# Optimization experiments

Measured on AMD Instinct MI355X. Metric: run time of the kernel, lower is better.

## Reference

```python
import jax, jax.numpy as jnp
import numpy as np

B, CIN, N, K, G, COUT = 8, 128, 2048, 16, 4, 256
NL = COUT // 4          # nl_channels = int(0.25*out_channels) = 64
L = COUT - NL           # l_channels = 192
CL = L // G             # 48 per local head
CNL = NL // G           # 16 per non-local head


def setup_inputs() -> dict:
    key = jax.random.key(0)
    ks = jax.random.split(key, 16)
    s = 0.05
    r = lambda k_, sh: s * jax.random.normal(k_, sh, jnp.float32)
    return {
        "x": jax.random.normal(ks[0], (B, CIN, N, K), jnp.float32),
        "abs_x": jax.random.normal(ks[1], (B, CIN // 2, N, 1), jnp.float32),
        "points": jax.random.normal(ks[2], (B, 3, N), jnp.float32),
        "Wq": r(ks[3], (L, CIN // 2)),
        "Wk": r(ks[4], (L, CIN // 2)),
        "Wv": r(ks[5], (L, CIN)),
        "Wnq": r(ks[6], (NL, CIN // 2)),
        "Wnk": r(ks[7], (NL, CIN // 2)),
        "Wnv1": r(ks[8], (NL, CIN // 2)),
        "Wnv2": r(ks[9], (NL, CIN // 2)),
        "pe_w1": r(ks[10], (3, L)),
        "pe_b1": jnp.zeros((L,), jnp.float32),
        "pe_w2": r(ks[11], (L, L)),
        "pe_b2": jnp.zeros((L,), jnp.float32),
        "npe_w1": r(ks[12], (G, 3, CNL)),
        "npe_b1": jnp.zeros((G, CNL), jnp.float32),
        "npe_w2": r(ks[13], (G, CNL, CNL)),
        "npe_b2": jnp.zeros((G, CNL), jnp.float32),
        "idx": jax.random.randint(ks[14], (B, 1, N, K), 0, N, dtype=jnp.int32),
    }


def _forward(x, abs_x, points, Wq, Wk, Wv, Wnq, Wnk, Wnv1, Wnv2,
             pe_w1, pe_b1, pe_w2, pe_b2, npe_w1, npe_b1, npe_w2, npe_b2, idx):
    b, c, n, k = x.shape
    half = c // 2
    idx_sq = idx[:, 0]                                   # (b,n,k)

    # ---- 1. Local attention over kNN neighbors ----
    lq = jnp.einsum('oc,bcns->bons', Wq, abs_x).reshape(b, G, CL, n, 1)
    lk = jnp.einsum('oc,bcnk->bonk', Wk, x[:, half:] + x[:, :half]).reshape(b, G, CL, n, k)
    lv = jnp.einsum('oc,bcnk->bonk', Wv, x).reshape(b, G, CL, n, k)

    # absolute positional encoding (select_neighbors -> carte MLP)
    nbr = jax.vmap(lambda p, i: p[:, i])(points, idx_sq)  # (b,3,n,k)
    rel = nbr - nbr[..., 0:1]                             # subtract first neighbor
    h = jax.nn.relu(jnp.einsum('bcnk,cd->bnkd', rel, pe_w1) + pe_b1)
    pe = (jnp.einsum('bnkd,de->bnke', h, pe_w2) + pe_b2).transpose(0, 3, 1, 2)
    lk = lk + pe.reshape(b, G, CL, n, k)

    att = jax.nn.softmax((lq * lk).sum(2), axis=-1)       # (b,G,n,k)
    local_feature = jnp.einsum('bgnk,bgcnk->bgcn', att, lv).reshape(b, L, n, 1)

    # ---- scatter-based sparse attention centrality + top-k node selection ----
    idx_flat = idx_sq.reshape(b, n * k)
    att_flat = att.reshape(b, G, n * k)

    def scat(a_g, i):  # a_g: (G, n*k), i: (n*k,)
        return jax.vmap(lambda a: jnp.zeros((n,), a.dtype).at[i].add(a))(a_g)

    cent = jax.vmap(scat)(att_flat, idx_flat)             # (b,G,n)
    vals, inds = jax.lax.top_k(cent, k)                   # (b,G,k)

    # ---- 2. Non-local MHA over selected nodes ----
    a2 = abs_x[..., 0]                                    # (b,half,n)
    nq = jnp.einsum('oc,bcn->bon', Wnq, a2).reshape(b, G, CNL, n)
    nk_ = jnp.einsum('oc,bcn->bon', Wnk, a2).reshape(b, G, CNL, n)
    nv1 = jnp.einsum('oc,bcn->bon', Wnv1, a2).reshape(b, G, CNL, n)
    nv2 = jnp.einsum('oc,bcn->bon', Wnv2, a2).reshape(b, G, CNL, n)

    gi = inds[:, :, None, :]                              # (b,G,1,k)
    nk_sel = jnp.take_along_axis(nk_, gi, axis=3)         # (b,G,CNL,k)
    nv2j = jnp.take_along_axis(nv2, gi, axis=3)           # (b,G,CNL,k)

    # per-group non-local positional encoding (constant over n by construction)
    sel = jnp.take_along_axis(jnp.broadcast_to(points[:, None], (b, G, 3, n)), gi, axis=3)  # (b,G,3,k)
    rel_nl = sel - sel[..., 0:1]
    h2 = jax.nn.relu(jnp.einsum('bgck,gcd->bgkd', rel_nl, npe_w1) + npe_b1[None, :, None, :])
    pe_nl = (jnp.einsum('bgkd,gde->bgke', h2, npe_w2) + npe_b2[None, :, None, :]).transpose(0, 1, 3, 2)  # (b,G,CNL,k)

    att_nl = jax.nn.softmax(jnp.einsum('bgcn,bgck->bgnk', nq, nk_sel + pe_nl), axis=-1)
    # value[b,g,c,n,k] = nv1[...,n] - nv2[...,n] + nv2j[...,k], gated by tanh(centrality)
    w = att_nl * jnp.tanh(vals)[:, :, None, :]            # (b,G,n,k)
    s = w.sum(-1)                                         # (b,G,n)
    nl_feature = (nv1 - nv2) * s[:, :, None, :] + jnp.einsum('bgnk,bgck->bgcn', w, nv2j)
    nl_feature = nl_feature.reshape(b, NL, n, 1)

    return jnp.concatenate([local_feature, nl_feature], axis=1)  # (b,COUT,n,1)


def reference(x, abs_x, points, Wq, Wk, Wv, Wnq, Wnk, Wnv1, Wnv2,
              pe_w1, pe_b1, pe_w2, pe_b2, npe_w1, npe_b1, npe_w2, npe_b2, idx):
    return _forward(x, abs_x, points, Wq, Wk, Wv, Wnq, Wnk, Wnv1, Wnv2,
                    pe_w1, pe_b1, pe_w2, pe_b2, npe_w1, npe_b1, npe_w2, npe_b2, idx)
```

## Files before the change

kernel.cpp:

```cpp
#include <hip/hip_runtime.h>
#include <cstddef>

constexpr int NN = 2048;
constexpr int GG = 4;

__global__ __launch_bounds__(256) void prep_q(const float* __restrict__ Wq,
                                              const float* __restrict__ Wk,
                                              const float* __restrict__ pe_w2,
                                              float* __restrict__ Qbuf) {
    const int g = blockIdx.x >> 6, c2 = blockIdx.x & 63;
    const int row = threadIdx.x;
    float acc = 0.f;
    if (row < 64) {
        for (int j = 0; j < 48; ++j) {
            const int o = g * 48 + j;
            acc = fmaf(Wk[o * 64 + row], Wq[o * 64 + c2], acc);
        }
    } else {
        const int d = row - 64;
        for (int j = 0; j < 48; ++j) {
            const int o = g * 48 + j;
            acc = fmaf(pe_w2[(size_t)d * 192 + o], Wq[o * 64 + c2], acc);
        }
    }
    Qbuf[((size_t)(g * 64 + c2) << 8) + row] = acc;
}

__global__ __launch_bounds__(256, 3) void local_v7c(
    const float* __restrict__ x, const float* __restrict__ abs_x,
    const float* __restrict__ points, const float* __restrict__ Wv,
    const float* __restrict__ pe_w1, const float* __restrict__ pe_b1,
    const int* __restrict__ idx, const float* __restrict__ Qbuf,
    float* __restrict__ out, float* __restrict__ cent)
{
    const int bn = blockIdx.x;
    const int b  = bn >> 8;
    const int n0 = (bn & 255) << 3;
    const int tid = threadIdx.x;

    __shared__ int   sidx[128];
    __shared__ float sa2[64][8];
    __shared__ __align__(16) float s_big[4224];
    __shared__ float spart[128][9];
    __shared__ float s_small[544];

    float* sq   = s_big;
    float* sw2  = s_big;
    float* sxw  = s_big;
    float* spts = s_small;
    float* satt = s_small;

    if (tid < 128) sidx[tid] = idx[((size_t)b * NN + n0) * 16 + tid];
    for (int i = tid; i < 512; i += 256) {
        int c = i >> 3, nl = i & 7;
        sa2[c][nl] = abs_x[((size_t)b * 64 + c) * NN + n0 + nl];
    }
    __syncthreads();

    for (int i = tid; i < 384; i += 256) {
        int c3 = i >> 7, r = i & 127;
        spts[(c3 * 8 + (r >> 4)) * 16 + (r & 15)] =
            points[((size_t)b * 3 + c3) * NN + sidx[r]];
    }
    {
        const int g = tid >> 6, row = tid & 63;
        const float* qb = Qbuf + (((size_t)g * 64) << 8) + row;
        float a0 = 0.f, a1 = 0.f, a2v = 0.f, a3 = 0.f,
              a4 = 0.f, a5 = 0.f, a6 = 0.f, a7 = 0.f;
        for (int c2 = 0; c2 < 64; ++c2) {
            const float qv = qb[c2 << 8];
            const float4 v0 = *(const float4*)&sa2[c2][0];
            const float4 v1 = *(const float4*)&sa2[c2][4];
            a0 = fmaf(qv, v0.x, a0); a1 = fmaf(qv, v0.y, a1);
            a2v = fmaf(qv, v0.z, a2v); a3 = fmaf(qv, v0.w, a3);
            a4 = fmaf(qv, v1.x, a4); a5 = fmaf(qv, v1.y, a5);
            a6 = fmaf(qv, v1.z, a6); a7 = fmaf(qv, v1.w, a7);
        }
        const int base = (g << 3) * 65 + row;
        sq[base + 0 * 65] = a0; sq[base + 1 * 65] = a1;
        sq[base + 2 * 65] = a2v; sq[base + 3 * 65] = a3;
        sq[base + 4 * 65] = a4; sq[base + 5 * 65] = a5;
        sq[base + 6 * 65] = a6; sq[base + 7 * 65] = a7;
    }
    __syncthreads();

    const int col = tid & 127, dh = tid >> 7;
    const int nlc = col >> 4, kkc = col & 15;

    {
        const float* xp = x + (((size_t)(b * 128 + dh * 32) * NN) + n0 + nlc) * 16 + kkc;
        const float* q0 = &sq[((0 << 3) + nlc) * 65 + dh * 32];
        const float* q1 = &sq[((1 << 3) + nlc) * 65 + dh * 32];
        const float* q2 = &sq[((2 << 3) + nlc) * 65 + dh * 32];
        const float* q3 = &sq[((3 << 3) + nlc) * 65 + dh * 32];
        float a0 = 0.f, a1 = 0.f, a2v = 0.f, a3 = 0.f;
        for (int i = 0; i < 32; ++i) {
            const float xs = xp[0] + xp[(size_t)64 * NN * 16];
            xp += NN * 16;
            a0 = fmaf(q0[i], xs, a0);
            a1 = fmaf(q1[i], xs, a1);
            a2v = fmaf(q2[i], xs, a2v);
            a3 = fmaf(q3[i], xs, a3);
        }
        spart[col][dh * 4 + 0] = a0; spart[col][dh * 4 + 1] = a1;
        spart[col][dh * 4 + 2] = a2v; spart[col][dh * 4 + 3] = a3;
    }
    __syncthreads();

    const float r0 = spts[(0 * 8 + nlc) * 16 + kkc] - spts[(0 * 8 + nlc) * 16];
    const float r1 = spts[(1 * 8 + nlc) * 16 + kkc] - spts[(1 * 8 + nlc) * 16];
    const float r2 = spts[(2 * 8 + nlc) * 16 + kkc] - spts[(2 * 8 + nlc) * 16];
    #pragma unroll
    for (int p = 0; p < 2; ++p) {
        if (tid < 192) {
            const int d = tid;
            float w00=0.f,w01=0.f,w02=0.f,w03=0.f,w04=0.f,w05=0.f,w06=0.f,w07=0.f;
            float w10=0.f,w11=0.f,w12=0.f,w13=0.f,w14=0.f,w15=0.f,w16=0.f,w17=0.f;
            const float* qb0 = Qbuf + (((size_t)(2 * p + 0) * 64) << 8) + 64 + d;
            const float* qb1 = Qbuf + (((size_t)(2 * p + 1) * 64) << 8) + 64 + d;
            for (int c2 = 0; c2 < 64; ++c2) {
                const float qv0 = qb0[c2 << 8];
                const float qv1 = qb1[c2 << 8];
                const float4 v0 = *(const float4*)&sa2[c2][0];
                const float4 v1 = *(const float4*)&sa2[c2][4];
                w00 = fmaf(qv0, v0.x, w00); w01 = fmaf(qv0, v0.y, w01);
                w02 = fmaf(qv0, v0.z, w02); w03 = fmaf(qv0, v0.w, w03);
                w04 = fmaf(qv0, v1.x, w04); w05 = fmaf(qv0, v1.y, w05);
                w06 = fmaf(qv0, v1.z, w06); w07 = fmaf(qv0, v1.w, w07);
                w10 = fmaf(qv1, v0.x, w10); w11 = fmaf(qv1, v0.y, w11);
                w12 = fmaf(qv1, v0.z, w12); w13 = fmaf(qv1, v0.w, w13);
                w14 = fmaf(qv1, v1.x, w14); w15 = fmaf(qv1, v1.y, w15);
                w16 = fmaf(qv1, v1.z, w16); w17 = fmaf(qv1, v1.w, w17);
            }
            sw2[(0 * 8 + 0) * 196 + d] = w00; sw2[(0 * 8 + 1) * 196 + d] = w01;
            sw2[(0 * 8 + 2) * 196 + d] = w02; sw2[(0 * 8 + 3) * 196 + d] = w03;
            sw2[(0 * 8 + 4) * 196 + d] = w04; sw2[(0 * 8 + 5) * 196 + d] = w05;
            sw2[(0 * 8 + 6) * 196 + d] = w06; sw2[(0 * 8 + 7) * 196 + d] = w07;
            sw2[(1 * 8 + 0) * 196 + d] = w10; sw2[(1 * 8 + 1) * 196 + d] = w11;
            sw2[(1 * 8 + 2) * 196 + d] = w12; sw2[(1 * 8 + 3) * 196 + d] = w13;
            sw2[(1 * 8 + 4) * 196 + d] = w14; sw2[(1 * 8 + 5) * 196 + d] = w15;
            sw2[(1 * 8 + 6) * 196 + d] = w16; sw2[(1 * 8 + 7) * 196 + d] = w17;
        }
        __syncthreads();
        {
            float pB0 = 0.f, pB1 = 0.f;
            const float* w0 = &sw2[(0 * 8 + nlc) * 196];
            const float* w1 = &sw2[(1 * 8 + nlc) * 196];
            const int d0 = dh * 96;
            for (int d = d0; d < d0 + 96; d += 4) {
                const float4 w1a = *(const float4*)&pe_w1[d];
                const float4 w1b = *(const float4*)&pe_w1[192 + d];
                const float4 w1c = *(const float4*)&pe_w1[384 + d];
                const float4 bb  = *(const float4*)&pe_b1[d];
                const float h0 = fmaxf(fmaf(r0, w1a.x, fmaf(r1, w1b.x, fmaf(r2, w1c.x, bb.x))), 0.f);
                const float h1 = fmaxf(fmaf(r0, w1a.y, fmaf(r1, w1b.y, fmaf(r2, w1c.y, bb.y))), 0.f);
                const float h2 = fmaxf(fmaf(r0, w1a.z, fmaf(r1, w1b.z, fmaf(r2, w1c.z, bb.z))), 0.f);
                const float h3 = fmaxf(fmaf(r0, w1a.w, fmaf(r1, w1b.w, fmaf(r2, w1c.w, bb.w))), 0.f);
                const float4 wa = *(const float4*)&w0[d];
                const float4 wb = *(const float4*)&w1[d];
                pB0 = fmaf(h0, wa.x, fmaf(h1, wa.y, fmaf(h2, wa.z, fmaf(h3, wa.w, pB0))));
                pB1 = fmaf(h0, wb.x, fmaf(h1, wb.y, fmaf(h2, wb.z, fmaf(h3, wb.w, pB1))));
            }
            spart[col][dh * 4 + 2 * p + 0] += pB0;
            spart[col][dh * 4 + 2 * p + 1] += pB1;
        }
        __syncthreads();
    }

    if (tid < 32) {
        const int g = tid >> 3, nl = tid & 7;
        float lg[16], m = -1e30f;
        #pragma unroll
        for (int kk = 0; kk < 16; ++kk) {
            const int cc = nl * 16 + kk;
            lg[kk] = spart[cc][g] + spart[cc][4 + g];
            m = fmaxf(m, lg[kk]);
        }
        float s = 0.f;
        #pragma unroll
        for (int kk = 0; kk < 16; ++kk) { lg[kk] = __expf(lg[kk] - m); s += lg[kk]; }
        const float inv = 1.f / s;
        #pragma unroll
        for (int kk = 0; kk < 16; ++kk) satt[nl * 68 + g * 16 + kk] = lg[kk] * inv;
    }
    __syncthreads();

    #pragma unroll
    for (int t = 0; t < 4; ++t) {
        const int i2 = t * 256 + tid;
        const int c = i2 >> 3, nl = i2 & 7;
        const float* xp = x + (((size_t)(b * 128 + c) * NN) + n0 + nl) * 16;
        const float4 x0 = *(const float4*)(xp);
        const float4 x1 = *(const float4*)(xp + 4);
        const float4 x2 = *(const float4*)(xp + 8);
        const float4 x3 = *(const float4*)(xp + 12);
        const float* at = &satt[nl * 68];
        #pragma unroll
        for (int g = 0; g < 4; ++g) {
            const float* a = at + g * 16;
            float v = 0.f;
            v = fmaf(x0.x, a[0],  v); v = fmaf(x0.y, a[1],  v);
            v = fmaf(x0.z, a[2],  v); v = fmaf(x0.w, a[3],  v);
            v = fmaf(x1.x, a[4],  v); v = fmaf(x1.y, a[5],  v);
            v = fmaf(x1.z, a[6],  v); v = fmaf(x1.w, a[7],  v);
            v = fmaf(x2.x, a[8],  v); v = fmaf(x2.y, a[9],  v);
            v = fmaf(x2.z, a[10], v); v = fmaf(x2.w, a[11], v);
            v = fmaf(x3.x, a[12], v); v = fmaf(x3.y, a[13], v);
            v = fmaf(x3.z, a[14], v); v = fmaf(x3.w, a[15], v);
            sxw[((g << 3) + nl) * 132 + c] = v;
        }
    }
    __syncthreads();

    #pragma unroll
    for (int rep = 0; rep < 6; ++rep) {
        const int i = rep * 256 + tid;
        const int o = i >> 3, nl = i & 7;
        const int g = o / 48;
        const float* wv  = Wv + (size_t)o * 128;
        const float* xwp = &sxw[((g << 3) + nl) * 132];
        float a = 0.f;
        for (int c = 0; c < 128; c += 4) {
            const float4 w4  = *(const float4*)(wv + c);
            const float4 xw4 = *(const float4*)(xwp + c);
            a = fmaf(w4.x, xw4.x, fmaf(w4.y, xw4.y, fmaf(w4.z, xw4.z, fmaf(w4.w, xw4.w, a))));
        }
        out[(((size_t)b << 8) + o) * NN + n0 + nl] = a;
    }

    if (tid < 32) {
        const int g = tid >> 3, nl = tid & 7;
        #pragma unroll
        for (int kk = 0; kk < 16; ++kk)
            atomicAdd(&cent[((size_t)(b * GG + g) << 11) + sidx[nl * 16 + kk]],
                      satt[nl * 68 + g * 16 + kk]);
    }
}

__global__ __launch_bounds__(512) void topk_prep_kernel(
    const float* __restrict__ abs_x, const float* __restrict__ points,
    const float* __restrict__ Wnk, const float* __restrict__ Wnv2,
    const float* __restrict__ npe_w1, const float* __restrict__ npe_b1,
    const float* __restrict__ npe_w2, const float* __restrict__ npe_b2,
    const float* __restrict__ cent,
    float* __restrict__ nkpe, float* __restrict__ nv2j, float* __restrict__ tanhv)
{
    const int bg  = blockIdx.x;
    const int b   = bg >> 2, g = bg & 3;
    const int tid = threadIdx.x;
    __shared__ float sc[2048];
    __shared__ float rv[8];  __shared__ int ri[8];
    __shared__ float svals[16]; __shared__ int sinds[16];
    __shared__ float srel[3][16];
    __shared__ float sh2[16][16];

    for (int i = tid; i < 2048; i += 512) sc[i] = cent[((size_t)bg << 11) + i];
    __syncthreads();
    for (int t = 0; t < 16; ++t) {
        float bv = -1e30f; int bi = 1 << 30;
        for (int i = tid; i < 2048; i += 512) {
            float v = sc[i];
            if (v > bv) { bv = v; bi = i; }
        }
        #pragma unroll
        for (int off = 1; off < 64; off <<= 1) {
            float ov = __shfl_xor(bv, off, 64);
            int   oi = __shfl_xor(bi, off, 64);
            if (ov > bv || (ov == bv && oi < bi)) { bv = ov; bi = oi; }
        }
        if ((tid & 63) == 0) { rv[tid >> 6] = bv; ri[tid >> 6] = bi; }
        __syncthreads();
        if (tid == 0) {
            for (int w = 1; w < 8; ++w)
                if (rv[w] > bv || (rv[w] == bv && ri[w] < bi)) { bv = rv[w]; bi = ri[w]; }
            svals[t] = bv; sinds[t] = bi;
            sc[bi] = -1e30f;
        }
        __syncthreads();
    }

    if (tid < 48) {
        int c = tid >> 4, j = tid & 15;
        srel[c][j] = points[((size_t)b * 3 + c) * NN + sinds[j]]
                   - points[((size_t)b * 3 + c) * NN + sinds[0]];
    }
    __syncthreads();
    if (tid < 256) {
        int j = tid >> 4, d = tid & 15;
        float a = npe_b1[g * 16 + d];
        #pragma unroll
        for (int c = 0; c < 3; ++c) a = fmaf(srel[c][j], npe_w1[((g * 3 + c) << 4) + d], a);
        sh2[j][d] = fmaxf(a, 0.f);
    }
    __syncthreads();
    if (tid < 256) {
        int c = tid >> 4, j = tid & 15;
        float a = npe_b2[g * 16 + c];
        #pragma unroll
        for (int d = 0; d < 16; ++d) a = fmaf(sh2[j][d], npe_w2[((g * 16 + d) << 4) + c], a);
        float nk = 0.f, nv = 0.f;
        const int colj = sinds[j];
        const float* a2  = abs_x + (size_t)b * 64 * NN + colj;
        const float* wkr = Wnk  + ((size_t)(g * 16 + c) << 6);
        const float* wvr = Wnv2 + ((size_t)(g * 16 + c) << 6);
        for (int ci = 0; ci < 64; ++ci) {
            float av = a2[(size_t)ci * NN];
            nk = fmaf(wkr[ci], av, nk);
            nv = fmaf(wvr[ci], av, nv);
        }
        nkpe[((size_t)bg << 8) + (c << 4) + j] = nk + a;
        nv2j[((size_t)bg << 8) + (c << 4) + j] = nv;
    }
    if (tid < 16) tanhv[(bg << 4) + tid] = tanhf(svals[tid]);
}

__global__ __launch_bounds__(256) void nonlocal_kernel(
    const float* __restrict__ abs_x,
    const float* __restrict__ Wnq, const float* __restrict__ Wnv1, const float* __restrict__ Wnv2,
    const float* __restrict__ nkpe, const float* __restrict__ nv2j, const float* __restrict__ tanhv,
    float* __restrict__ out)
{
    const int blk = blockIdx.x;
    const int b   = blk >> 5;
    const int n0  = (blk & 31) << 6;
    const int tid = threadIdx.x;
    const int nl  = tid & 63;
    const int g   = tid >> 6;

    __shared__ float sa2[64][64];
    __shared__ float snkpe[4][16][16];
    __shared__ float snv2j[4][16][16];
    __shared__ float stanh[4][16];

    for (int i = tid; i < 64 * 64; i += 256) {
        int ci = i >> 6, c2 = i & 63;
        sa2[ci][c2] = abs_x[((size_t)b * 64 + ci) * NN + n0 + c2];
    }
    for (int i = tid; i < 1024; i += 256) {
        ((float*)snkpe)[i] = nkpe[((size_t)b << 10) + i];
        ((float*)snv2j)[i] = nv2j[((size_t)b << 10) + i];
    }
    if (tid < 64) ((float*)stanh)[tid] = tanhv[(b << 6) + tid];
    __syncthreads();

    float nq[16], nv1[16], nv2[16];
    #pragma unroll
    for (int c = 0; c < 16; ++c) { nq[c] = 0.f; nv1[c] = 0.f; nv2[c] = 0.f; }
    const float* wq  = Wnq  + (size_t)(g << 4) * 64;
    const float* wv1 = Wnv1 + (size_t)(g << 4) * 64;
    const float* wv2 = Wnv2 + (size_t)(g << 4) * 64;
    for (int ci = 0; ci < 64; ++ci) {
        const float a = sa2[ci][nl];
        #pragma unroll
        for (int c = 0; c < 16; ++c) {
            nq[c]  = fmaf(wq [(c << 6) + ci], a, nq[c]);
            nv1[c] = fmaf(wv1[(c << 6) + ci], a, nv1[c]);
            nv2[c] = fmaf(wv2[(c << 6) + ci], a, nv2[c]);
        }
    }

    float lg[16];
    #pragma unroll
    for (int j = 0; j < 16; ++j) {
        float a = 0.f;
        #pragma unroll
        for (int c = 0; c < 16; ++c) a = fmaf(nq[c], snkpe[g][c][j], a);
        lg[j] = a;
    }
    float m = lg[0];
    #pragma unroll
    for (int j = 1; j < 16; ++j) m = fmaxf(m, lg[j]);
    float s = 0.f;
    float w[16];
    #pragma unroll
    for (int j = 0; j < 16; ++j) { w[j] = __expf(lg[j] - m); s += w[j]; }
    const float inv = 1.f / s;
    float ws = 0.f;
    #pragma unroll
    for (int j = 0; j < 16; ++j) { w[j] = w[j] * inv * stanh[g][j]; ws += w[j]; }
    #pragma unroll
    for (int c = 0; c < 16; ++c) {
        float v = (nv1[c] - nv2[c]) * ws;
        #pragma unroll
        for (int j = 0; j < 16; ++j) v = fmaf(w[j], snv2j[g][c][j], v);
        out[(((size_t)b << 8) + 192 + (g << 4) + c) * NN + n0 + nl] = v;
    }
}

extern "C" void kernel_launch(void* const* d_in, const int* in_sizes, int n_in,
                              void* d_out, int out_size, void* d_ws, size_t ws_size,
                              hipStream_t stream)
{
    (void)in_sizes; (void)n_in; (void)out_size; (void)ws_size;
    const float* x      = (const float*)d_in[0];
    const float* abs_x  = (const float*)d_in[1];
    const float* points = (const float*)d_in[2];
    const float* Wq     = (const float*)d_in[3];
    const float* Wk     = (const float*)d_in[4];
    const float* Wv     = (const float*)d_in[5];
    const float* Wnq    = (const float*)d_in[6];
    const float* Wnk    = (const float*)d_in[7];
    const float* Wnv1   = (const float*)d_in[8];
    const float* Wnv2   = (const float*)d_in[9];
    const float* pe_w1  = (const float*)d_in[10];
    const float* pe_b1  = (const float*)d_in[11];
    const float* pe_w2  = (const float*)d_in[12];
    const float* npe_w1 = (const float*)d_in[14];
    const float* npe_b1 = (const float*)d_in[15];
    const float* npe_w2 = (const float*)d_in[16];
    const float* npe_b2 = (const float*)d_in[17];
    const int*   idx    = (const int*)d_in[18];
    float* out = (float*)d_out;

    float* cent  = (float*)d_ws;
    float* Qbuf  = cent + 65536;
    float* nkpeW = Qbuf + 65536;
    float* nv2jW = nkpeW + 8192;
    float* tanhW = nv2jW + 8192;

    hipMemsetAsync(cent, 0, (size_t)65536 * sizeof(float), stream);
    prep_q<<<256, 256, 0, stream>>>(Wq, Wk, pe_w2, Qbuf);
    local_v7c<<<2048, 256, 0, stream>>>(x, abs_x, points, Wv, pe_w1, pe_b1,
                                        idx, Qbuf, out, cent);
    topk_prep_kernel<<<32, 512, 0, stream>>>(abs_x, points, Wnk, Wnv2,
                                             npe_w1, npe_b1, npe_w2, npe_b2,
                                             cent, nkpeW, nv2jW, tanhW);
    nonlocal_kernel<<<8 * 32, 256, 0, stream>>>(abs_x, Wnq, Wnv1, Wnv2,
                                                nkpeW, nv2jW, tanhW, out);
}
```

Measured before the change: 241.3 us.

## Batch global loads in local kernel, prefetch x tile, and use two-level top-k

In the local attention kernel, the Q, Qbuf and x reduction loops now issue eight or four global loads in a batch before their FMAs, so more memory requests are in flight at once. The x tile used by the later value stage is loaded into registers early, before the positional-encoding phase, so its latency overlaps that compute. The top-k kernel replaces 16 block-wide serial argmax passes, each with two barriers, with a per-wave top-16 followed by a single-wave merge of the 128 candidates. Holding 16 float4 values across the PE phase raises register pressure under the 3-blocks-per-SM launch bound and may cause spills.

```diff
diff --git a/kernel.cpp b/kernel.cpp
--- a/kernel.cpp
+++ b/kernel.cpp
@@ -26,7 +26,7 @@
     Qbuf[((size_t)(g * 64 + c2) << 8) + row] = acc;
 }
 
-__global__ __launch_bounds__(256, 3) void local_v7c(
+__global__ __launch_bounds__(256, 3) void local_v8(
     const float* __restrict__ x, const float* __restrict__ abs_x,
     const float* __restrict__ points, const float* __restrict__ Wv,
     const float* __restrict__ pe_w1, const float* __restrict__ pe_b1,
@@ -67,14 +67,19 @@
         const float* qb = Qbuf + (((size_t)g * 64) << 8) + row;
         float a0 = 0.f, a1 = 0.f, a2v = 0.f, a3 = 0.f,
               a4 = 0.f, a5 = 0.f, a6 = 0.f, a7 = 0.f;
-        for (int c2 = 0; c2 < 64; ++c2) {
-            const float qv = qb[c2 << 8];
-            const float4 v0 = *(const float4*)&sa2[c2][0];
-            const float4 v1 = *(const float4*)&sa2[c2][4];
-            a0 = fmaf(qv, v0.x, a0); a1 = fmaf(qv, v0.y, a1);
-            a2v = fmaf(qv, v0.z, a2v); a3 = fmaf(qv, v0.w, a3);
-            a4 = fmaf(qv, v1.x, a4); a5 = fmaf(qv, v1.y, a5);
-            a6 = fmaf(qv, v1.z, a6); a7 = fmaf(qv, v1.w, a7);
+        for (int c2 = 0; c2 < 64; c2 += 8) {
+            float qv[8];
+            #pragma unroll
+            for (int j = 0; j < 8; ++j) qv[j] = qb[(c2 + j) << 8];
+            #pragma unroll
+            for (int j = 0; j < 8; ++j) {
+                const float4 v0 = *(const float4*)&sa2[c2 + j][0];
+                const float4 v1 = *(const float4*)&sa2[c2 + j][4];
+                a0 = fmaf(qv[j], v0.x, a0); a1 = fmaf(qv[j], v0.y, a1);
+                a2v = fmaf(qv[j], v0.z, a2v); a3 = fmaf(qv[j], v0.w, a3);
+                a4 = fmaf(qv[j], v1.x, a4); a5 = fmaf(qv[j], v1.y, a5);
+                a6 = fmaf(qv[j], v1.z, a6); a7 = fmaf(qv[j], v1.w, a7);
+            }
         }
         const int base = (g << 3) * 65 + row;
         sq[base + 0 * 65] = a0; sq[base + 1 * 65] = a1;
@@ -89,21 +94,42 @@
 
     {
         const float* xp = x + (((size_t)(b * 128 + dh * 32) * NN) + n0 + nlc) * 16 + kkc;
+        const size_t cstr = (size_t)NN * 16;
         const float* q0 = &sq[((0 << 3) + nlc) * 65 + dh * 32];
         const float* q1 = &sq[((1 << 3) + nlc) * 65 + dh * 32];
         const float* q2 = &sq[((2 << 3) + nlc) * 65 + dh * 32];
         const float* q3 = &sq[((3 << 3) + nlc) * 65 + dh * 32];
         float a0 = 0.f, a1 = 0.f, a2v = 0.f, a3 = 0.f;
-        for (int i = 0; i < 32; ++i) {
-            const float xs = xp[0] + xp[(size_t)64 * NN * 16];
-            xp += NN * 16;
-            a0 = fmaf(q0[i], xs, a0);
-            a1 = fmaf(q1[i], xs, a1);
-            a2v = fmaf(q2[i], xs, a2v);
-            a3 = fmaf(q3[i], xs, a3);
+        for (int i0 = 0; i0 < 32; i0 += 8) {
+            float lo[8], hi[8];
+            #pragma unroll
+            for (int j = 0; j < 8; ++j) {
+                lo[j] = xp[(size_t)(i0 + j) * cstr];
+                hi[j] = xp[(size_t)(i0 + j + 64) * cstr];
+            }
+            #pragma unroll
+            for (int j = 0; j < 8; ++j) {
+                const float xs = lo[j] + hi[j];
+                a0 = fmaf(q0[i0 + j], xs, a0);
+                a1 = fmaf(q1[i0 + j], xs, a1);
+                a2v = fmaf(q2[i0 + j], xs, a2v);
+                a3 = fmaf(q3[i0 + j], xs, a3);
+            }
         }
         spart[col][dh * 4 + 0] = a0; spart[col][dh * 4 + 1] = a1;
         spart[col][dh * 4 + 2] = a2v; spart[col][dh * 4 + 3] = a3;
+    }
+
+    float4 xpre[16];
+    #pragma unroll
+    for (int t = 0; t < 4; ++t) {
+        const int i2 = t * 256 + tid;
+        const int c = i2 >> 3, nl = i2 & 7;
+        const float* xp4 = x + (((size_t)(b * 128 + c) * NN) + n0 + nl) * 16;
+        xpre[t * 4 + 0] = *(const float4*)(xp4);
+        xpre[t * 4 + 1] = *(const float4*)(xp4 + 4);
+        xpre[t * 4 + 2] = *(const float4*)(xp4 + 8);
+        xpre[t * 4 + 3] = *(const float4*)(xp4 + 12);
     }
     __syncthreads();
 
@@ -118,19 +144,26 @@
             float w10=0.f,w11=0.f,w12=0.f,w13=0.f,w14=0.f,w15=0.f,w16=0.f,w17=0.f;
             const float* qb0 = Qbuf + (((size_t)(2 * p + 0) * 64) << 8) + 64 + d;
             const float* qb1 = Qbuf + (((size_t)(2 * p + 1) * 64) << 8) + 64 + d;
-            for (int c2 = 0; c2 < 64; ++c2) {
-                const float qv0 = qb0[c2 << 8];
-                const float qv1 = qb1[c2 << 8];
-                const float4 v0 = *(const float4*)&sa2[c2][0];
-                const float4 v1 = *(const float4*)&sa2[c2][4];
-                w00 = fmaf(qv0, v0.x, w00); w01 = fmaf(qv0, v0.y, w01);
-                w02 = fmaf(qv0, v0.z, w02); w03 = fmaf(qv0, v0.w, w03);
-                w04 = fmaf(qv0, v1.x, w04); w05 = fmaf(qv0, v1.y, w05);
-                w06 = fmaf(qv0, v1.z, w06); w07 = fmaf(qv0, v1.w, w07);
-                w10 = fmaf(qv1, v0.x, w10); w11 = fmaf(qv1, v0.y, w11);
-                w12 = fmaf(qv1, v0.z, w12); w13 = fmaf(qv1, v0.w, w13);
-                w14 = fmaf(qv1, v1.x, w14); w15 = fmaf(qv1, v1.y, w15);
-                w16 = fmaf(qv1, v1.z, w16); w17 = fmaf(qv1, v1.w, w17);
+            for (int c2 = 0; c2 < 64; c2 += 4) {
+                float qv0[4], qv1[4];
+                #pragma unroll
+                for (int j = 0; j < 4; ++j) {
+                    qv0[j] = qb0[(c2 + j) << 8];
+                    qv1[j] = qb1[(c2 + j) << 8];
+                }
+                #pragma unroll
+                for (int j = 0; j < 4; ++j) {
+                    const float4 v0 = *(const float4*)&sa2[c2 + j][0];
+                    const float4 v1 = *(const float4*)&sa2[c2 + j][4];
+                    w00 = fmaf(qv0[j], v0.x, w00); w01 = fmaf(qv0[j], v0.y, w01);
+                    w02 = fmaf(qv0[j], v0.z, w02); w03 = fmaf(qv0[j], v0.w, w03);
+                    w04 = fmaf(qv0[j], v1.x, w04); w05 = fmaf(qv0[j], v1.y, w05);
+                    w06 = fmaf(qv0[j], v1.z, w06); w07 = fmaf(qv0[j], v1.w, w07);
+                    w10 = fmaf(qv1[j], v0.x, w10); w11 = fmaf(qv1[j], v0.y, w11);
+                    w12 = fmaf(qv1[j], v0.z, w12); w13 = fmaf(qv1[j], v0.w, w13);
+                    w14 = fmaf(qv1[j], v1.x, w14); w15 = fmaf(qv1[j], v1.y, w15);
+                    w16 = fmaf(qv1[j], v1.z, w16); w17 = fmaf(qv1[j], v1.w, w17);
+                }
             }
             sw2[(0 * 8 + 0) * 196 + d] = w00; sw2[(0 * 8 + 1) * 196 + d] = w01;
             sw2[(0 * 8 + 2) * 196 + d] = w02; sw2[(0 * 8 + 3) * 196 + d] = w03;
@@ -147,6 +180,7 @@
             const float* w0 = &sw2[(0 * 8 + nlc) * 196];
             const float* w1 = &sw2[(1 * 8 + nlc) * 196];
             const int d0 = dh * 96;
+            #pragma unroll 2
             for (int d = d0; d < d0 + 96; d += 4) {
                 const float4 w1a = *(const float4*)&pe_w1[d];
                 const float4 w1b = *(const float4*)&pe_w1[192 + d];
@@ -189,11 +223,10 @@
     for (int t = 0; t < 4; ++t) {
         const int i2 = t * 256 + tid;
         const int c = i2 >> 3, nl = i2 & 7;
-        const float* xp = x + (((size_t)(b * 128 + c) * NN) + n0 + nl) * 16;
-        const float4 x0 = *(const float4*)(xp);
-        const float4 x1 = *(const float4*)(xp + 4);
-        const float4 x2 = *(const float4*)(xp + 8);
-        const float4 x3 = *(const float4*)(xp + 12);
+        const float4 x0 = xpre[t * 4 + 0];
+        const float4 x1 = xpre[t * 4 + 1];
+        const float4 x2 = xpre[t * 4 + 2];
+        const float4 x3 = xpre[t * 4 + 3];
         const float* at = &satt[nl * 68];
         #pragma unroll
         for (int g = 0; g < 4; ++g) {
@@ -220,6 +253,7 @@
         const float* wv  = Wv + (size_t)o * 128;
         const float* xwp = &sxw[((g << 3) + nl) * 132];
         float a = 0.f;
+        #pragma unroll 8
         for (int c = 0; c < 128; c += 4) {
             const float4 w4  = *(const float4*)(wv + c);
             const float4 xw4 = *(const float4*)(xwp + c);
@@ -248,36 +282,63 @@
     const int bg  = blockIdx.x;
     const int b   = bg >> 2, g = bg & 3;
     const int tid = threadIdx.x;
+    const int wave = tid >> 6, lane = tid & 63;
     __shared__ float sc[2048];
-    __shared__ float rv[8];  __shared__ int ri[8];
+    __shared__ float cval[128]; __shared__ int cidx[128];
     __shared__ float svals[16]; __shared__ int sinds[16];
     __shared__ float srel[3][16];
     __shared__ float sh2[16][16];
 
     for (int i = tid; i < 2048; i += 512) sc[i] = cent[((size_t)bg << 11) + i];
     __syncthreads();
-    for (int t = 0; t < 16; ++t) {
-        float bv = -1e30f; int bi = 1 << 30;
-        for (int i = tid; i < 2048; i += 512) {
-            float v = sc[i];
-            if (v > bv) { bv = v; bi = i; }
-        }
-        #pragma unroll
-        for (int off = 1; off < 64; off <<= 1) {
-            float ov = __shfl_xor(bv, off, 64);
-            int   oi = __shfl_xor(bi, off, 64);
-            if (ov > bv || (ov == bv && oi < bi)) { bv = ov; bi = oi; }
-        }
-        if ((tid & 63) == 0) { rv[tid >> 6] = bv; ri[tid >> 6] = bi; }
-        __syncthreads();
-        if (tid == 0) {
-            for (int w = 1; w < 8; ++w)
-                if (rv[w] > bv || (rv[w] == bv && ri[w] < bi)) { bv = rv[w]; bi = ri[w]; }
-            svals[t] = bv; sinds[t] = bi;
-            sc[bi] = -1e30f;
-        }
-        __syncthreads();
-    }
+
+    {
+        float v[4]; int ix[4];
+        #pragma unroll
+        for (int j = 0; j < 4; ++j) {
+            const int i = wave * 256 + j * 64 + lane;
+            v[j] = sc[i]; ix[j] = i;
+        }
+        for (int t = 0; t < 16; ++t) {
+            float bv = v[0]; int bi = ix[0];
+            #pragma unroll
+            for (int j = 1; j < 4; ++j)
+                if (v[j] > bv || (v[j] == bv && ix[j] < bi)) { bv = v[j]; bi = ix[j]; }
+            float wv_ = bv; int wi_ = bi;
+            #pragma unroll
+            for (int off = 1; off < 64; off <<= 1) {
+                const float ov = __shfl_xor(wv_, off, 64);
+                const int   oi = __shfl_xor(wi_, off, 64);
+                if (ov > wv_ || (ov == wv_ && oi < wi_)) { wv_ = ov; wi_ = oi; }
+            }
+            #pragma unroll
+            for (int j = 0; j < 4; ++j)
+                if (ix[j] == wi_) { v[j] = -1e30f; ix[j] = 1 << 30; }
+            if (lane == 0) { cval[wave * 16 + t] = wv_; cidx[wave * 16 + t] = wi_; }
+        }
+    }
+    __syncthreads();
+
+    if (wave == 0) {
+        float m0 = cval[lane], m1 = cval[64 + lane];
+        int   j0 = cidx[lane], j1 = cidx[64 + lane];
+        for (int t = 0; t < 16; ++t) {
+            float bv; int bi;
+            if (m0 > m1 || (m0 == m1 && j0 < j1)) { bv = m0; bi = j0; }
+            else { bv = m1; bi = j1; }
+            float wv_ = bv; int wi_ = bi;
+            #pragma unroll
+            for (int off = 1; off < 64; off <<= 1) {
+                const float ov = __shfl_xor(wv_, off, 64);
+                const int   oi = __shfl_xor(wi_, off, 64);
+                if (ov > wv_ || (ov == wv_ && oi < wi_)) { wv_ = ov; wi_ = oi; }
+            }
+            if (j0 == wi_) { m0 = -1e30f; j0 = 1 << 30; }
+            if (j1 == wi_) { m1 = -1e30f; j1 = 1 << 30; }
+            if (lane == 0) { svals[t] = wv_; sinds[t] = wi_; }
+        }
+    }
+    __syncthreads();
 
     if (tid < 48) {
         int c = tid >> 4, j = tid & 15;
@@ -420,8 +481,8 @@
 
     hipMemsetAsync(cent, 0, (size_t)65536 * sizeof(float), stream);
     prep_q<<<256, 256, 0, stream>>>(Wq, Wk, pe_w2, Qbuf);
-    local_v7c<<<2048, 256, 0, stream>>>(x, abs_x, points, Wv, pe_w1, pe_b1,
-                                        idx, Qbuf, out, cent);
+    local_v8<<<2048, 256, 0, stream>>>(x, abs_x, points, Wv, pe_w1, pe_b1,
+                                       idx, Qbuf, out, cent);
     topk_prep_kernel<<<32, 512, 0, stream>>>(abs_x, points, Wnk, Wnv2,
                                              npe_w1, npe_b1, npe_w2, npe_b2,
                                              cent, nkpeW, nv2jW, tanhW);
```

Result: slower. 251.6 us (+4.3%).
